# Optimization experiments

Hardware: AMD Instinct MI355X
Metric: run time of the kernel (lower is better)

Reference implementation:

```python
import jax, jax.numpy as jnp
import numpy as np

B, Q, D, H, CTX, W_OUT = 2048, 256, 64, 128, 5, 32


def setup_inputs() -> dict:
    key = jax.random.key(0)
    ks = jax.random.split(key, 20)
    s = 0.05
    p = lambda k, shape: jax.random.normal(k, shape, dtype=jnp.float32) * s
    return {
        "x_in": jax.random.normal(ks[0], (B, Q, D), dtype=jnp.float32),
        "w_out": W_OUT,
        "conv_w": p(ks[1], (H, 3 * D, CTX)),
        "conv_b": p(ks[2], (H,)),
        "fc1_w": p(ks[3], (H, H)),
        "fc1_b": p(ks[4], (H,)),
        "fc2_w": p(ks[5], (D, H)),
        "fc2_b": p(ks[6], (D,)),
        "rot1_w": p(ks[7], (H, D)),
        "rot1_b": p(ks[8], (H,)),
        "rot2_w": p(ks[9], (2, H)),
        "rot2_b": p(ks[10], (2,)),
        "gru_wih": p(ks[11], (3 * H, D)),
        "gru_whh": p(ks[12], (3 * H, H)),
        "gru_bih": p(ks[13], (3 * H,)),
        "gru_bhh": p(ks[14], (3 * H,)),
        "out_w": p(ks[15], (D, H)),
        "out_b": p(ks[16], (D,)),
    }


def reference(x_in, w_out, conv_w, conv_b, fc1_w, fc1_b, fc2_w, fc2_b,
              rot1_w, rot1_b, rot2_w, rot2_b, gru_wih, gru_whh,
              gru_bih, gru_bhh, out_w, out_b):
    b, q, d = x_in.shape
    h_dim = fc1_w.shape[0]
    ctx = conv_w.shape[2]
    m = d // 2
    pi = np.float32(np.pi)

    def kalman_step(carry, y_t):
        x_post, y_prev, buf = carry
        # rotation params from posterior state
        rp = jnp.maximum(x_post @ rot1_w.T + rot1_b, 0.0) @ rot2_w.T + rot2_b
        rho = jax.nn.sigmoid(rp[:, 0:1]) * 1.5
        phi = jnp.tanh(rp[:, 1:2]) * pi
        # complex polar rotation: (a+ib) * rho*e^{i phi}
        a, bb = x_post[:, :m], x_post[:, m:]
        c = rho * jnp.cos(phi)
        s = rho * jnp.sin(phi)
        x_pri = jnp.concatenate([a * c - bb * s, a * s + bb * c], axis=1)
        innov = y_t - x_pri
        diff = y_t - y_prev
        feat = jnp.concatenate([innov, x_post, diff], axis=1)  # (B, 3D)
        # roll context buffer, append newest features
        buf = jnp.concatenate([buf[:, :, 1:], feat[:, :, None]], axis=2)
        # Conv1d(kernel=context, pad=0) over a context-length buffer == full contraction
        t = jnp.einsum('hck,bck->bh', conv_w, buf) + conv_b
        t = jnp.maximum(t, 0.0)
        t = jnp.maximum(t @ fc1_w.T + fc1_b, 0.0)
        K = jax.nn.sigmoid(t @ fc2_w.T + fc2_b)  # (B, D)
        x_post_new = x_pri + K * innov
        return (x_post_new, y_t, buf), None

    init = (jnp.zeros((b, d), x_in.dtype),
            x_in[:, 0, :],
            jnp.zeros((b, 3 * d, ctx), x_in.dtype))
    (x_post, _, _), _ = jax.lax.scan(kalman_step, init, jnp.swapaxes(x_in, 0, 1))

    def gru_step(carry, _):
        h, curr = carry
        gi = curr @ gru_wih.T + gru_bih
        gh = h @ gru_whh.T + gru_bhh
        i_r, i_z, i_n = jnp.split(gi, 3, axis=1)
        h_r, h_z, h_n = jnp.split(gh, 3, axis=1)
        r = jax.nn.sigmoid(i_r + h_r)
        z = jax.nn.sigmoid(i_z + h_z)
        n = jnp.tanh(i_n + r * h_n)
        h_new = (1.0 - z) * n + z * h
        curr_new = curr + (h_new @ out_w.T + out_b)
        return (h_new, curr_new), curr_new

    (_, _), preds = jax.lax.scan(
        gru_step, (jnp.zeros((b, h_dim), x_in.dtype), x_post), None, length=w_out)
    return jnp.swapaxes(preds, 0, 1)  # (B, w_out, D)
```

## Files before the change

### kernel.cpp

```cpp
#include <hip/hip_runtime.h>

#define QLEN 256
#define DDIM 64
#define WOUT 32

typedef __bf16 b8v __attribute__((ext_vector_type(8)));
typedef float f4v __attribute__((ext_vector_type(4)));

__device__ __forceinline__ f4v MFMA(b8v a, b8v b, f4v c) {
  return __builtin_amdgcn_mfma_f32_16x16x32_bf16(a, b, c, 0, 0, 0);
}
__device__ __forceinline__ float sigmoidf_(float x) { return 1.0f/(1.0f+__expf(-x)); }
__device__ __forceinline__ float tanhf_(float x)    { return 1.0f - 2.0f/(__expf(2.0f*x)+1.0f); }
__device__ __forceinline__ b8v lda(const __bf16* p, const __bf16* zp, bool pr) {
  return *(const b8v*)(pr ? p : zp);
}

__global__ __launch_bounds__(512, 2)
void k_kalman(const float* __restrict__ x_in,
              const float* __restrict__ conv_w, const float* __restrict__ conv_b,
              const float* __restrict__ fc1_w,  const float* __restrict__ fc1_b,
              const float* __restrict__ fc2_w,  const float* __restrict__ fc2_b,
              const float* __restrict__ rot1_w, const float* __restrict__ rot1_b,
              const float* __restrict__ rot2_w, const float* __restrict__ rot2_b,
              float* __restrict__ out)
{
  __shared__ __align__(16) __bf16 SMB[11872];
  __shared__ __align__(16) float  SMF[2560];
  const int tid = threadIdx.x;
  const int w  = tid >> 6;
  const int l  = tid & 63;
  const int lr = l & 15;
  const int lg = l >> 4;
  const int wg = blockIdx.x;
  const bool lo  = (w < 4);
  const bool pr8 = (lr < 8);

  __bf16* XPB  = SMB;
  __bf16* T1   = SMB + 576;
  __bf16* TC   = SMB + 1664;
  __bf16* T2   = SMB + 2752;
  __bf16* FEAT = SMB + 3840;
  const __bf16* ZP = SMB + 11840;
  float*  XPF  = SMF;
  float*  XPRI = SMF + 512;
  float*  INV  = SMF + 1024;
  float*  PART = SMF + 1536;

  for (int i = tid; i < 11872; i += 512) SMB[i] = (__bf16)0.0f;
  for (int i = tid; i < 2560;  i += 512) SMF[i] = 0.0f;

  const int hcol = 16*w + lr;
  const int tlo  = 2*(w & 3);

  constexpr int LO_CH[15] = {2,3,6,7,8,9,10,11,12,13,14, 0,1,4,5};

  b8v r1B[2], f1B[4], f2B[4], cvB[15][2];
  #pragma unroll
  for (int q = 0; q < 2; ++q)
    #pragma unroll
    for (int j = 0; j < 8; ++j)
      r1B[q][j] = (__bf16)rot1_w[hcol*64 + q*32 + lg*8 + j];
  #pragma unroll
  for (int q = 0; q < 4; ++q)
    #pragma unroll
    for (int j = 0; j < 8; ++j)
      f1B[q][j] = (__bf16)fc1_w[hcol*128 + q*32 + lg*8 + j];
  {
    const int h2 = lo ? hcol : 0;
    #pragma unroll
    for (int q = 0; q < 4; ++q)
      #pragma unroll
      for (int j = 0; j < 8; ++j)
        f2B[q][j] = (__bf16)fc2_w[h2*128 + q*32 + lg*8 + j];
  }
  #pragma unroll
  for (int i = 0; i < 15; ++i) {
    const int c = lo ? LO_CH[i] : (15 + i);
    const int L = c/6, q = c%6;
    #pragma unroll
    for (int ti = 0; ti < 2; ++ti)
      #pragma unroll
      for (int j = 0; j < 8; ++j)
        cvB[i][ti][j] =
          (__bf16)conv_w[((tlo+ti)*16 + lr)*960 + (q*32 + lg*8 + j)*5 + (4-L)];
  }

  const float b_r1 = rot1_b[hcol];
  const float b_f1 = fc1_b[hcol];
  const float b_f2 = fc2_b[lo ? hcol : 0];
  const float bc0  = conv_b[tlo*16 + lr];
  const float bc1  = conv_b[(tlo+1)*16 + lr];
  const float r2w00 = rot2_w[l],       r2w01 = rot2_w[64 + l];
  const float r2w10 = rot2_w[128 + l], r2w11 = rot2_w[192 + l];
  const float rb0 = rot2_b[0], rb1 = rot2_b[1];
  const float PI_F = 3.14159274f;

  const float* xptr = x_in + ((long)(wg*8 + w)*QLEN)*DDIM + l;
  float y_cur = xptr[0];
  float y_prv = y_cur;
  int slot = 0;

  __syncthreads();

  for (int t = 0; t < QLEN; ++t) {
    {
      b8v a0 = lda(&XPB[lr*72      + lg*8], ZP, pr8);
      b8v a1 = lda(&XPB[lr*72 + 32 + lg*8], ZP, pr8);
      f4v C = {};
      C = MFMA(a0, r1B[0], C);
      C = MFMA(a1, r1B[1], C);
      if (lg < 2) {
        #pragma unroll
        for (int r = 0; r < 4; ++r) {
          float v = C[r] + b_r1; v = v > 0.f ? v : 0.f;
          T1[(lg*4+r)*136 + hcol] = (__bf16)v;
        }
      }
    }
    __syncthreads();

    float t1a = (float)T1[w*136 + l];
    float t1b = (float)T1[w*136 + 64 + l];
    float y_nxt = (t+1 < QLEN) ? xptr[(t+1)*DDIM] : y_cur;
    f4v C0a = {}, C0b = {}, C1a = {}, C1b = {};
    if (lo) {
      #pragma unroll
      for (int i = 0; i < 11; ++i) {
        const int c = LO_CH[i], L = c/6, q = c%6;
        int s5 = slot - L; if (s5 < 0) s5 += 5;
        b8v a = lda(&FEAT[s5*1600 + lr*200 + q*32 + lg*8], ZP, pr8);
        if (i & 1) { C0b = MFMA(a, cvB[i][0], C0b); C1b = MFMA(a, cvB[i][1], C1b); }
        else       { C0a = MFMA(a, cvB[i][0], C0a); C1a = MFMA(a, cvB[i][1], C1a); }
      }
    } else {
      #pragma unroll
      for (int i = 0; i < 15; ++i) {
        const int c = 15+i, L = c/6, q = c%6;
        int s5 = slot - L; if (s5 < 0) s5 += 5;
        b8v a = lda(&FEAT[s5*1600 + lr*200 + q*32 + lg*8], ZP, pr8);
        if (i & 1) { C0b = MFMA(a, cvB[i][0], C0b); C1b = MFMA(a, cvB[i][1], C1b); }
        else       { C0a = MFMA(a, cvB[i][0], C0a); C1a = MFMA(a, cvB[i][1], C1a); }
      }
    }
    {
      float acc0 = t1a*r2w00 + t1b*r2w01;
      float acc1 = t1a*r2w10 + t1b*r2w11;
      #pragma unroll
      for (int m = 1; m < 64; m <<= 1) {
        acc0 += __shfl_xor(acc0, m, 64);
        acc1 += __shfl_xor(acc1, m, 64);
      }
      float rho = 1.5f * sigmoidf_(acc0 + rb0);
      float phi = PI_F * tanhf_(acc1 + rb1);
      float cc = rho * __cosf(phi);
      float ss = rho * __sinf(phi);
      float lo32 = XPF[w*64 + (l & 31)];
      float hi32 = XPF[w*64 + (l & 31) + 32];
      float xpri = (l < 32) ? (lo32*cc - hi32*ss) : (lo32*ss + hi32*cc);
      float innov = y_cur - xpri;
      float diff  = y_cur - y_prv;
      __bf16* fr = FEAT + slot*1600 + w*200;
      fr[l]       = (__bf16)innov;
      fr[128 + l] = (__bf16)diff;
      XPRI[w*64 + l] = xpri;
      INV [w*64 + l] = innov;
    }
    if (!lo && lg < 2) {
      f4v s0 = C0a + C0b, s1 = C1a + C1b;
      *(f4v*)&PART[tlo*128     + lr*8 + lg*4] = s0;
      *(f4v*)&PART[(tlo+1)*128 + lr*8 + lg*4] = s1;
    }
    __syncthreads();

    if (lo) {
      #pragma unroll
      for (int i = 11; i < 15; ++i) {
        const int q = LO_CH[i] % 6;
        b8v a = lda(&FEAT[slot*1600 + lr*200 + q*32 + lg*8], ZP, pr8);
        if (i & 1) { C0b = MFMA(a, cvB[i][0], C0b); C1b = MFMA(a, cvB[i][1], C1b); }
        else       { C0a = MFMA(a, cvB[i][0], C0a); C1a = MFMA(a, cvB[i][1], C1a); }
      }
      if (lg < 2) {
        f4v p0 = *(const f4v*)&PART[tlo*128     + lr*8 + lg*4];
        f4v p1 = *(const f4v*)&PART[(tlo+1)*128 + lr*8 + lg*4];
        #pragma unroll
        for (int r = 0; r < 4; ++r) {
          float v0 = C0a[r] + C0b[r] + p0[r] + bc0; v0 = v0 > 0.f ? v0 : 0.f;
          float v1 = C1a[r] + C1b[r] + p1[r] + bc1; v1 = v1 > 0.f ? v1 : 0.f;
          TC[(lg*4+r)*136 + tlo*16 + lr]     = (__bf16)v0;
          TC[(lg*4+r)*136 + (tlo+1)*16 + lr] = (__bf16)v1;
        }
      }
    }
    __syncthreads();

    {
      f4v D0 = {}, D1 = {};
      #pragma unroll
      for (int q = 0; q < 4; ++q) {
        b8v a = lda(&TC[lr*136 + q*32 + lg*8], ZP, pr8);
        if (q & 1) D1 = MFMA(a, f1B[q], D1); else D0 = MFMA(a, f1B[q], D0);
      }
      if (lg < 2) {
        #pragma unroll
        for (int r = 0; r < 4; ++r) {
          float v = D0[r] + D1[r] + b_f1; v = v > 0.f ? v : 0.f;
          T2[(lg*4+r)*136 + hcol] = (__bf16)v;
        }
      }
    }
    __syncthreads();

    const int slot_next = (slot == 4) ? 0 : slot + 1;
    if (lo) {
      f4v D0 = {}, D1 = {};
      #pragma unroll
      for (int q = 0; q < 4; ++q) {
        b8v a = lda(&T2[lr*136 + q*32 + lg*8], ZP, pr8);
        if (q & 1) D1 = MFMA(a, f2B[q], D1); else D0 = MFMA(a, f2B[q], D0);
      }
      if (lg < 2) {
        #pragma unroll
        for (int r = 0; r < 4; ++r) {
          int e = lg*4 + r;
          float K = sigmoidf_(D0[r] + D1[r] + b_f2);
          float xn = XPRI[e*64 + hcol] + K * INV[e*64 + hcol];
          XPF[e*64 + hcol] = xn;
          XPB[e*72 + hcol] = (__bf16)xn;
          FEAT[slot_next*1600 + e*200 + 64 + hcol] = (__bf16)xn;
        }
      }
    }
    __syncthreads();

    y_prv = y_cur; y_cur = y_nxt;
    slot = slot_next;
  }

  out[((long)(wg*8 + w)*WOUT)*DDIM + l] = XPF[w*64 + l];
}

__global__ __launch_bounds__(512, 2)
void k_gru(const float* __restrict__ gru_wih, const float* __restrict__ gru_whh,
           const float* __restrict__ gru_bih, const float* __restrict__ gru_bhh,
           const float* __restrict__ out_w,   const float* __restrict__ out_b,
           float* __restrict__ out)
{
  __shared__ __align__(16) __bf16 CUR[16*72];
  __shared__ __align__(16) __bf16 HB [16*136];
  const int tid = threadIdx.x;
  const int w  = tid >> 6, l = tid & 63, lr = l & 15, lg = l >> 4;
  const int g = blockIdx.x;

  for (int i = tid; i < 16*136; i += 512) HB[i] = (__bf16)0.f;
  for (int i = tid; i < 16*64; i += 512) {
    int e = i >> 6, d = i & 63;
    CUR[e*72 + d] = (__bf16)out[((long)(g*16 + e)*WOUT)*DDIM + d];
  }

  b8v fih[3][2], fhh[3][4], fo[4];
  #pragma unroll
  for (int n3 = 0; n3 < 3; ++n3) {
    int row = 16*(w + 8*n3) + lr;
    #pragma unroll
    for (int q = 0; q < 2; ++q)
      #pragma unroll
      for (int j = 0; j < 8; ++j)
        fih[n3][q][j] = (__bf16)gru_wih[row*64 + q*32 + lg*8 + j];
    #pragma unroll
    for (int q = 0; q < 4; ++q)
      #pragma unroll
      for (int j = 0; j < 8; ++j)
        fhh[n3][q][j] = (__bf16)gru_whh[row*128 + q*32 + lg*8 + j];
  }
  {
    int row = 16*(w & 3) + lr;
    #pragma unroll
    for (int q = 0; q < 4; ++q)
      #pragma unroll
      for (int j = 0; j < 8; ++j)
        fo[q][j] = (__bf16)out_w[row*128 + q*32 + lg*8 + j];
  }
  const int jh = 16*w + lr;
  const float b_ir = gru_bih[jh], b_iz = gru_bih[128+jh], b_in = gru_bih[256+jh];
  const float b_hr = gru_bhh[jh], b_hz = gru_bhh[128+jh], b_hn = gru_bhh[256+jh];
  const float b_o  = out_b[16*(w & 3) + lr];
  const int dcol = 16*(w & 3) + lr;
  __syncthreads();

  for (int s = 0; s < WOUT; ++s) {
    f4v cI[3] = {}, cH[3] = {};
    #pragma unroll
    for (int q = 0; q < 2; ++q) {
      b8v a = *(const b8v*)&CUR[lr*72 + q*32 + lg*8];
      #pragma unroll
      for (int n3 = 0; n3 < 3; ++n3) cI[n3] = MFMA(a, fih[n3][q], cI[n3]);
    }
    #pragma unroll
    for (int q = 0; q < 4; ++q) {
      b8v a = *(const b8v*)&HB[lr*136 + q*32 + lg*8];
      #pragma unroll
      for (int n3 = 0; n3 < 3; ++n3) cH[n3] = MFMA(a, fhh[n3][q], cH[n3]);
    }
    __syncthreads();

    #pragma unroll
    for (int r = 0; r < 4; ++r) {
      int e = lg*4 + r;
      float ir = cI[0][r] + b_ir, iz = cI[1][r] + b_iz, in_ = cI[2][r] + b_in;
      float hr = cH[0][r] + b_hr, hz = cH[1][r] + b_hz, hn  = cH[2][r] + b_hn;
      float rr = sigmoidf_(ir + hr);
      float zz = sigmoidf_(iz + hz);
      float nn = tanhf_(in_ + rr*hn);
      float hold = (float)HB[e*136 + jh];
      float hnew = (1.f - zz)*nn + zz*hold;
      HB[e*136 + jh] = (__bf16)hnew;
    }
    __syncthreads();

    if (w < 4) {
      f4v C0 = {};
      #pragma unroll
      for (int q = 0; q < 4; ++q) {
        b8v a = *(const b8v*)&HB[lr*136 + q*32 + lg*8];
        C0 = MFMA(a, fo[q], C0);
      }
      #pragma unroll
      for (int r = 0; r < 4; ++r) {
        int e = lg*4 + r;
        float cn = (float)CUR[e*72 + dcol] + C0[r] + b_o;
        CUR[e*72 + dcol] = (__bf16)cn;
        out[(((long)(g*16 + e))*WOUT + s)*DDIM + dcol] = cn;
      }
    }
    __syncthreads();
  }
}

extern "C" void kernel_launch(void* const* d_in, const int* in_sizes, int n_in,
                              void* d_out, int out_size, void* d_ws, size_t ws_size,
                              hipStream_t stream) {
  (void)in_sizes; (void)n_in; (void)d_ws; (void)ws_size; (void)out_size;
  const float* x_in   = (const float*)d_in[0];
  const float* conv_w = (const float*)d_in[2];
  const float* conv_b = (const float*)d_in[3];
  const float* fc1_w  = (const float*)d_in[4];
  const float* fc1_b  = (const float*)d_in[5];
  const float* fc2_w  = (const float*)d_in[6];
  const float* fc2_b  = (const float*)d_in[7];
  const float* rot1_w = (const float*)d_in[8];
  const float* rot1_b = (const float*)d_in[9];
  const float* rot2_w = (const float*)d_in[10];
  const float* rot2_b = (const float*)d_in[11];
  const float* gwih   = (const float*)d_in[12];
  const float* gwhh   = (const float*)d_in[13];
  const float* gbih   = (const float*)d_in[14];
  const float* gbhh   = (const float*)d_in[15];
  const float* ow     = (const float*)d_in[16];
  const float* ob     = (const float*)d_in[17];
  float* out = (float*)d_out;

  k_kalman<<<256, 512, 0, stream>>>(x_in, conv_w, conv_b, fc1_w, fc1_b,
                                    fc2_w, fc2_b, rot1_w, rot1_b,
                                    rot2_w, rot2_b, out);
  k_gru<<<128, 512, 0, stream>>>(gwih, gwhh, gbih, gbhh, ow, ob, out);
}
```

Before: 737.9 us.

## Give each wave its own conv output columns and spread GRU across more blocks

The Kalman conv stage previously had the eight waves split the 30 input chunks and pass partial sums through shared memory. It now gives each wave its own 16 output columns over all 30 chunks, which removes the partial-sum buffer and its cross-wave combine. Each wave now holds 30 bf16 weight fragments instead of 30 paired ones, so register pressure stays similar, but it issues more serial MFMAs per wave. The GRU kernel now runs 256 blocks with 8 batch rows each instead of 128 blocks with 16, padding the MFMA tile with zero rows. This raises occupancy at the cost of wasted MFMA lanes.

```diff
diff --git a/kernel.cpp b/kernel.cpp
--- a/kernel.cpp
+++ b/kernel.cpp
@@ -26,14 +26,13 @@
               float* __restrict__ out)
 {
   __shared__ __align__(16) __bf16 SMB[11872];
-  __shared__ __align__(16) float  SMF[2560];
+  __shared__ __align__(16) float  SMF[1536];
   const int tid = threadIdx.x;
   const int w  = tid >> 6;
   const int l  = tid & 63;
   const int lr = l & 15;
   const int lg = l >> 4;
   const int wg = blockIdx.x;
-  const bool lo  = (w < 4);
   const bool pr8 = (lr < 8);
 
   __bf16* XPB  = SMB;
@@ -45,17 +44,13 @@
   float*  XPF  = SMF;
   float*  XPRI = SMF + 512;
   float*  INV  = SMF + 1024;
-  float*  PART = SMF + 1536;
 
   for (int i = tid; i < 11872; i += 512) SMB[i] = (__bf16)0.0f;
-  for (int i = tid; i < 2560;  i += 512) SMF[i] = 0.0f;
+  for (int i = tid; i < 1536;  i += 512) SMF[i] = 0.0f;
 
   const int hcol = 16*w + lr;
-  const int tlo  = 2*(w & 3);
-
-  constexpr int LO_CH[15] = {2,3,6,7,8,9,10,11,12,13,14, 0,1,4,5};
-
-  b8v r1B[2], f1B[4], f2B[4], cvB[15][2];
+
+  b8v r1B[2], f1B[4], f2B[4], cvB[30];
   #pragma unroll
   for (int q = 0; q < 2; ++q)
     #pragma unroll
@@ -67,7 +62,7 @@
     for (int j = 0; j < 8; ++j)
       f1B[q][j] = (__bf16)fc1_w[hcol*128 + q*32 + lg*8 + j];
   {
-    const int h2 = lo ? hcol : 0;
+    const int h2 = (w < 4) ? hcol : 0;
     #pragma unroll
     for (int q = 0; q < 4; ++q)
       #pragma unroll
@@ -75,22 +70,17 @@
         f2B[q][j] = (__bf16)fc2_w[h2*128 + q*32 + lg*8 + j];
   }
   #pragma unroll
-  for (int i = 0; i < 15; ++i) {
-    const int c = lo ? LO_CH[i] : (15 + i);
+  for (int c = 0; c < 30; ++c) {
     const int L = c/6, q = c%6;
     #pragma unroll
-    for (int ti = 0; ti < 2; ++ti)
-      #pragma unroll
-      for (int j = 0; j < 8; ++j)
-        cvB[i][ti][j] =
-          (__bf16)conv_w[((tlo+ti)*16 + lr)*960 + (q*32 + lg*8 + j)*5 + (4-L)];
+    for (int j = 0; j < 8; ++j)
+      cvB[c][j] = (__bf16)conv_w[hcol*960 + (q*32 + lg*8 + j)*5 + (4-L)];
   }
 
   const float b_r1 = rot1_b[hcol];
   const float b_f1 = fc1_b[hcol];
-  const float b_f2 = fc2_b[lo ? hcol : 0];
-  const float bc0  = conv_b[tlo*16 + lr];
-  const float bc1  = conv_b[(tlo+1)*16 + lr];
+  const float b_f2 = fc2_b[(w < 4) ? hcol : 0];
+  const float bc   = conv_b[hcol];
   const float r2w00 = rot2_w[l],       r2w01 = rot2_w[64 + l];
   const float r2w10 = rot2_w[128 + l], r2w11 = rot2_w[192 + l];
   const float rb0 = rot2_b[0], rb1 = rot2_b[1];
@@ -120,30 +110,24 @@
     }
     __syncthreads();
 
-    float t1a = (float)T1[w*136 + l];
-    float t1b = (float)T1[w*136 + 64 + l];
     float y_nxt = (t+1 < QLEN) ? xptr[(t+1)*DDIM] : y_cur;
-    f4v C0a = {}, C0b = {}, C1a = {}, C1b = {};
-    if (lo) {
-      #pragma unroll
-      for (int i = 0; i < 11; ++i) {
-        const int c = LO_CH[i], L = c/6, q = c%6;
-        int s5 = slot - L; if (s5 < 0) s5 += 5;
-        b8v a = lda(&FEAT[s5*1600 + lr*200 + q*32 + lg*8], ZP, pr8);
-        if (i & 1) { C0b = MFMA(a, cvB[i][0], C0b); C1b = MFMA(a, cvB[i][1], C1b); }
-        else       { C0a = MFMA(a, cvB[i][0], C0a); C1a = MFMA(a, cvB[i][1], C1a); }
-      }
-    } else {
-      #pragma unroll
-      for (int i = 0; i < 15; ++i) {
-        const int c = 15+i, L = c/6, q = c%6;
-        int s5 = slot - L; if (s5 < 0) s5 += 5;
-        b8v a = lda(&FEAT[s5*1600 + lr*200 + q*32 + lg*8], ZP, pr8);
-        if (i & 1) { C0b = MFMA(a, cvB[i][0], C0b); C1b = MFMA(a, cvB[i][1], C1b); }
-        else       { C0a = MFMA(a, cvB[i][0], C0a); C1a = MFMA(a, cvB[i][1], C1a); }
-      }
-    }
-    {
+    f4v Ca = {}, Cb = {};
+    {
+      const __bf16* fb1 = FEAT + ((slot-1+5)%5)*1600 + lr*200 + lg*8;
+      const __bf16* fb2 = FEAT + ((slot-2+5)%5)*1600 + lr*200 + lg*8;
+      const __bf16* fb3 = FEAT + ((slot-3+5)%5)*1600 + lr*200 + lg*8;
+      const __bf16* fb4 = FEAT + ((slot-4+5)%5)*1600 + lr*200 + lg*8;
+      #pragma unroll
+      for (int c = 6; c < 30; ++c) {
+        const int L = c/6, q = c%6;
+        const __bf16* fb = (L==1) ? fb1 : (L==2) ? fb2 : (L==3) ? fb3 : fb4;
+        b8v a = lda(&fb[q*32], ZP, pr8);
+        if (c & 1) Cb = MFMA(a, cvB[c], Cb); else Ca = MFMA(a, cvB[c], Ca);
+      }
+    }
+    {
+      float t1a = (float)T1[w*136 + l];
+      float t1b = (float)T1[w*136 + 64 + l];
       float acc0 = t1a*r2w00 + t1b*r2w01;
       float acc1 = t1a*r2w10 + t1b*r2w11;
       #pragma unroll
@@ -166,30 +150,20 @@
       XPRI[w*64 + l] = xpri;
       INV [w*64 + l] = innov;
     }
-    if (!lo && lg < 2) {
-      f4v s0 = C0a + C0b, s1 = C1a + C1b;
-      *(f4v*)&PART[tlo*128     + lr*8 + lg*4] = s0;
-      *(f4v*)&PART[(tlo+1)*128 + lr*8 + lg*4] = s1;
-    }
-    __syncthreads();
-
-    if (lo) {
-      #pragma unroll
-      for (int i = 11; i < 15; ++i) {
-        const int q = LO_CH[i] % 6;
-        b8v a = lda(&FEAT[slot*1600 + lr*200 + q*32 + lg*8], ZP, pr8);
-        if (i & 1) { C0b = MFMA(a, cvB[i][0], C0b); C1b = MFMA(a, cvB[i][1], C1b); }
-        else       { C0a = MFMA(a, cvB[i][0], C0a); C1a = MFMA(a, cvB[i][1], C1a); }
+    __syncthreads();
+
+    {
+      const __bf16* fb0 = FEAT + slot*1600 + lr*200 + lg*8;
+      #pragma unroll
+      for (int c = 0; c < 6; ++c) {
+        b8v a = lda(&fb0[c*32], ZP, pr8);
+        if (c & 1) Cb = MFMA(a, cvB[c], Cb); else Ca = MFMA(a, cvB[c], Ca);
       }
       if (lg < 2) {
-        f4v p0 = *(const f4v*)&PART[tlo*128     + lr*8 + lg*4];
-        f4v p1 = *(const f4v*)&PART[(tlo+1)*128 + lr*8 + lg*4];
         #pragma unroll
         for (int r = 0; r < 4; ++r) {
-          float v0 = C0a[r] + C0b[r] + p0[r] + bc0; v0 = v0 > 0.f ? v0 : 0.f;
-          float v1 = C1a[r] + C1b[r] + p1[r] + bc1; v1 = v1 > 0.f ? v1 : 0.f;
-          TC[(lg*4+r)*136 + tlo*16 + lr]     = (__bf16)v0;
-          TC[(lg*4+r)*136 + (tlo+1)*16 + lr] = (__bf16)v1;
+          float v = Ca[r] + Cb[r] + bc; v = v > 0.f ? v : 0.f;
+          TC[(lg*4+r)*136 + hcol] = (__bf16)v;
         }
       }
     }
@@ -213,7 +187,7 @@
     __syncthreads();
 
     const int slot_next = (slot == 4) ? 0 : slot + 1;
-    if (lo) {
+    if (w < 4) {
       f4v D0 = {}, D1 = {};
       #pragma unroll
       for (int q = 0; q < 4; ++q) {
@@ -254,9 +228,11 @@
   const int g = blockIdx.x;
 
   for (int i = tid; i < 16*136; i += 512) HB[i] = (__bf16)0.f;
-  for (int i = tid; i < 16*64; i += 512) {
+  for (int i = tid; i < 16*72; i += 512) CUR[i] = (__bf16)0.f;
+  __syncthreads();
+  for (int i = tid; i < 8*64; i += 512) {
     int e = i >> 6, d = i & 63;
-    CUR[e*72 + d] = (__bf16)out[((long)(g*16 + e)*WOUT)*DDIM + d];
+    CUR[e*72 + d] = (__bf16)out[((long)(g*8 + e)*WOUT)*DDIM + d];
   }
 
   b8v fih[3][2], fhh[3][4], fo[4];
@@ -331,7 +307,8 @@
         int e = lg*4 + r;
         float cn = (float)CUR[e*72 + dcol] + C0[r] + b_o;
         CUR[e*72 + dcol] = (__bf16)cn;
-        out[(((long)(g*16 + e))*WOUT + s)*DDIM + dcol] = cn;
+        if (e < 8)
+          out[(((long)(g*8 + e))*WOUT + s)*DDIM + dcol] = cn;
       }
     }
     __syncthreads();
@@ -364,5 +341,5 @@
   k_kalman<<<256, 512, 0, stream>>>(x_in, conv_w, conv_b, fc1_w, fc1_b,
                                     fc2_w, fc2_b, rot1_w, rot1_b,
                                     rot2_w, rot2_b, out);
-  k_gru<<<128, 512, 0, stream>>>(gwih, gwhh, gbih, gbhh, ow, ob, out);
-}
+  k_gru<<<256, 512, 0, stream>>>(gwih, gwhh, gbih, gbhh, ow, ob, out);
+}
```

After: 692.6 us. 6.1% less time.
